# Optimization experiments

Hardware: AMD Instinct MI355X
Metric: run time of the kernel (lower is better)

## Reference

```python
import jax, jax.numpy as jnp
import numpy as np

B, C, H, W = 8, 256, 64, 64   # batch, num_hiddens, spatial
N, D = 1024, 256              # n_embed, embedding_dim
TEMP = 1.0                    # temp_init


def setup_inputs() -> dict:
    key = jax.random.key(0)
    k1, k2, k3 = jax.random.split(key, 3)
    z = jax.random.normal(k1, (B, C, H, W), dtype=jnp.float32)
    # 1x1 conv == per-pixel linear: weight [n_embed, num_hiddens], bias [n_embed]
    proj_w = jax.random.normal(k2, (N, C), dtype=jnp.float32) * 0.02
    proj_b = jnp.zeros((N,), dtype=jnp.float32)
    embed = jax.random.normal(k3, (N, D), dtype=jnp.float32) * 0.02
    return {"z": z, "proj_w": proj_w, "proj_b": proj_b, "embed": embed}


def reference(z, proj_w, proj_b, embed):
    # logits = Conv2d(num_hiddens, n_embed, 1)(z)  -> [b, n, h, w]
    logits = jnp.einsum('bchw,nc->bnhw', z, proj_w) + proj_b[None, :, None, None]
    # argmax_softmax (straight-through) over the codebook axis (dim=1), tau=TEMP
    y_soft = jax.nn.softmax(logits / TEMP, axis=1)
    ind = jnp.argmax(y_soft, axis=1)  # [b, h, w]
    y_hard = jax.nn.one_hot(ind, N, axis=1, dtype=logits.dtype)  # [b, n, h, w]
    soft_one_hot = y_hard - jax.lax.stop_gradient(y_soft) + y_soft
    # z_q = einsum('b n h w, n d -> b d h w', soft_one_hot, embed)
    z_q = jnp.einsum('bnhw,nd->bdhw', soft_one_hot, embed)
    diff = jnp.zeros((1,), dtype=logits.dtype)
    return (z_q, diff, ind)
```

## Files before the change

kernel.cpp:

```cpp
#include <hip/hip_runtime.h>
#include <math.h>

#define HWP 4096
#define CCH 256
#define NN  1024
#define DD  256
#define ZQ_SIZE (8 * DD * HWP)
#define MARGIN 1e-4f
#define WLCAP 4096

typedef _Float16 h8 __attribute__((ext_vector_type(8)));
typedef float    f4 __attribute__((ext_vector_type(4)));

__global__ __launch_bounds__(256) void split_w_k(
    const float* __restrict__ w, _Float16* __restrict__ whS, _Float16* __restrict__ wlS,
    int* __restrict__ wcount)
{
    if (blockIdx.x == 0 && threadIdx.x == 0) *wcount = 0;
    const int t = blockIdx.x * 256 + threadIdx.x;
    const int l = t & 63;
    const int frag = t >> 6;
    const int kc = frag & 7, r16 = frag >> 3;
    const int row = r16 * 16 + (l & 15);
    const int c   = kc * 32 + (l >> 4) * 8;
    const float* src = w + (size_t)row * CCH + c;
    _Float16 hv[8], lv[8];
#pragma unroll
    for (int j = 0; j < 8; ++j) {
        const float x = src[j];
        const _Float16 h = (_Float16)x;
        hv[j] = h;
        lv[j] = (_Float16)(x - (float)h);
    }
    *(h8*)(whS + (size_t)t * 8) = *(const h8*)hv;
    *(h8*)(wlS + (size_t)t * 8) = *(const h8*)lv;
}

__global__ __launch_bounds__(256, 2) void mfma_gemm_k(
    const float* __restrict__ z,
    const _Float16* __restrict__ whS, const _Float16* __restrict__ wlS,
    const float* __restrict__ bias, const float* __restrict__ embed,
    int* __restrict__ wcount, int* __restrict__ wlist,
    float* __restrict__ out)
{
    __shared__ __align__(16) char smem[68608];
    __shared__ int indsh2[64];
    float* s_best = (float*)(smem + 65536);
    float* s_sec  = (float*)(smem + 66560);
    int*   s_idx  = (int*)  (smem + 67584);

    const int tid = threadIdx.x;
    const int l   = tid & 63;
    const int wv  = tid >> 6;
    const int c15 = l & 15, g = l >> 4;
    const int pix0 = blockIdx.x * 64;
    const int b = pix0 >> 12, p0 = pix0 & 4095;

    {
        const int px = tid & 63;
        const int p16 = px >> 4;
        const float* zb = z + (size_t)b * CCH * HWP + p0 + px;
#pragma unroll
        for (int it = 0; it < 8; ++it) {
            const int cg = wv * 8 + it;
            const int c = cg * 8;
            float xv[8];
#pragma unroll
            for (int i = 0; i < 8; ++i) xv[i] = zb[(size_t)(c + i) * HWP];
            _Float16 hv[8], lv[8];
#pragma unroll
            for (int i = 0; i < 8; ++i) {
                const _Float16 h = (_Float16)xv[i];
                hv[i] = h;
                lv[i] = (_Float16)(xv[i] - (float)h);
            }
            const int kc = cg >> 2;
            const int lane = (px & 15) + 16 * (cg & 3);
            const int off = ((p16 * 8 + kc) * 64 + lane) * 16;
            *(h8*)(smem + off)         = *(const h8*)hv;
            *(h8*)(smem + 32768 + off) = *(const h8*)lv;
        }
    }
    __syncthreads();

    float best[16], sec[16]; int bidx[16];
#pragma unroll
    for (int s = 0; s < 16; ++s) { best[s] = -INFINITY; sec[s] = -INFINITY; bidx[s] = 0; }

#pragma unroll 1
    for (int nt = 0; nt < 4; ++nt) {
        const int n0 = nt * 256 + wv * 64;
        const int r16_0 = n0 >> 4;
        f4 acc[4][4];
#pragma unroll
        for (int mf = 0; mf < 4; ++mf)
#pragma unroll
            for (int nf = 0; nf < 4; ++nf) acc[mf][nf] = (f4)0.f;

#pragma unroll 2
        for (int kc = 0; kc < 8; ++kc) {
            h8 ah[4], al[4], bh[4], bl[4];
#pragma unroll
            for (int mf = 0; mf < 4; ++mf) {
                const int ao = ((mf * 8 + kc) * 64 + l) * 16;
                ah[mf] = *(const h8*)(smem + ao);
                al[mf] = *(const h8*)(smem + 32768 + ao);
            }
#pragma unroll
            for (int nf = 0; nf < 4; ++nf) {
                const size_t bo = (((size_t)(r16_0 + nf) * 8 + kc) * 64 + l) * 8;
                bh[nf] = *(const h8*)(whS + bo);
                bl[nf] = *(const h8*)(wlS + bo);
            }
#pragma unroll
            for (int mf = 0; mf < 4; ++mf)
#pragma unroll
                for (int nf = 0; nf < 4; ++nf) {
                    acc[mf][nf] = __builtin_amdgcn_mfma_f32_16x16x32_f16(ah[mf], bh[nf], acc[mf][nf], 0, 0, 0);
                    acc[mf][nf] = __builtin_amdgcn_mfma_f32_16x16x32_f16(ah[mf], bl[nf], acc[mf][nf], 0, 0, 0);
                    acc[mf][nf] = __builtin_amdgcn_mfma_f32_16x16x32_f16(al[mf], bh[nf], acc[mf][nf], 0, 0, 0);
                }
        }
#pragma unroll
        for (int nf = 0; nf < 4; ++nf) {
            const int n_abs = n0 + nf * 16 + c15;
            const float bv = bias[n_abs];
#pragma unroll
            for (int mf = 0; mf < 4; ++mf)
#pragma unroll
                for (int r = 0; r < 4; ++r) {
                    const float v = acc[mf][nf][r] + bv;
                    const int s = mf * 4 + r;
                    if (v > best[s]) { sec[s] = best[s]; best[s] = v; bidx[s] = n_abs; }
                    else if (v > sec[s]) sec[s] = v;
                }
        }
    }

#pragma unroll
    for (int d = 1; d < 16; d <<= 1) {
#pragma unroll
        for (int s = 0; s < 16; ++s) {
            const float ob = __shfl_xor(best[s], d, 64);
            const float os = __shfl_xor(sec[s], d, 64);
            const int   oi = __shfl_xor(bidx[s], d, 64);
            if (ob > best[s])       { sec[s] = fmaxf(best[s], os); best[s] = ob; bidx[s] = oi; }
            else if (ob == best[s]) { sec[s] = ob; bidx[s] = (oi < bidx[s]) ? oi : bidx[s]; }
            else                    { sec[s] = fmaxf(sec[s], ob); }
        }
    }
#pragma unroll
    for (int s = 0; s < 16; ++s) {
        if (c15 == s) {
            const int px = (s >> 2) * 16 + g * 4 + (s & 3);
            s_best[wv * 64 + px] = best[s];
            s_sec [wv * 64 + px] = sec[s];
            s_idx [wv * 64 + px] = bidx[s];
        }
    }
    __syncthreads();
    if (tid < 64) {
        float b0 = s_best[tid], s0 = s_sec[tid]; int i0 = s_idx[tid];
#pragma unroll
        for (int c = 1; c < 4; ++c) {
            const float ob = s_best[c * 64 + tid], os = s_sec[c * 64 + tid];
            const int   oi = s_idx[c * 64 + tid];
            if (ob > b0 || (ob == b0 && oi < i0)) { s0 = fmaxf(b0, os); b0 = ob; i0 = oi; }
            else                                  { s0 = fmaxf(s0, ob); }
        }
        const int pix = pix0 + tid;
        indsh2[tid] = i0;
        out[ZQ_SIZE + 1 + pix] = (float)i0;
        if (b0 - s0 < MARGIN) {
            const int pos = atomicAdd(wcount, 1);
            if (pos < WLCAP) wlist[pos] = pix;
        }
    }
    if (blockIdx.x == 0 && tid == 0) out[ZQ_SIZE] = 0.0f;
    __syncthreads();

    float (*tile)[257] = (float (*)[257])smem;
    const int lq = tid & 63, wq = tid >> 6;
    const int l32 = tid & 31, dq = tid >> 5;
#pragma unroll 1
    for (int pp = 0; pp < 2; ++pp) {
#pragma unroll
        for (int it = 0; it < 8; ++it) {
            const int pl = it * 4 + wq;
            const int row = indsh2[pp * 32 + pl];
            const float4 e = *(const float4*)(embed + (size_t)row * DD + lq * 4);
            tile[pl][lq * 4 + 0] = e.x;
            tile[pl][lq * 4 + 1] = e.y;
            tile[pl][lq * 4 + 2] = e.z;
            tile[pl][lq * 4 + 3] = e.w;
        }
        __syncthreads();
        float* outz = out + (size_t)b * DD * HWP + p0 + pp * 32;
#pragma unroll
        for (int dd = 0; dd < 32; ++dd) {
            const int d = dd * 8 + dq;
            outz[(size_t)d * HWP + l32] = tile[l32][d];
        }
        __syncthreads();
    }
}

__global__ __launch_bounds__(256) void fixup_k(
    const float* __restrict__ z, const float* __restrict__ w,
    const float* __restrict__ bias, const float* __restrict__ embed,
    const int* __restrict__ wcount, const int* __restrict__ wlist,
    float* __restrict__ out)
{
    __shared__ float zsh[256];
    __shared__ float m_v[4];
    __shared__ int   m_i[4];
    __shared__ int   s_i;

    const int tid = threadIdx.x;
    const int l = tid & 63, wv = tid >> 6;
    const int c15 = l & 15, q = l >> 4;
    int nw = *wcount;
    if (nw > WLCAP) nw = WLCAP;

    for (int e = blockIdx.x; e < nw; e += 256) {
        const int pix = wlist[e];
        const int b = pix >> 12, p = pix & 4095;
        __syncthreads();
        zsh[tid] = z[((size_t)b * CCH + tid) * HWP + p];
        __syncthreads();

        float best = -INFINITY; int bi = 0;
        for (int g16 = 0; g16 < 16; ++g16) {
            const int row = wv * 256 + g16 * 16 + c15;
            const float* wr = w + (size_t)row * CCH + q * 64;
            float part = 0.f;
#pragma unroll
            for (int j = 0; j < 16; ++j) {
                const float4 w4 = *(const float4*)(wr + j * 4);
                const float4 z4 = *(const float4*)&zsh[q * 64 + j * 4];
                part = fmaf(w4.x, z4.x, part);
                part = fmaf(w4.y, z4.y, part);
                part = fmaf(w4.z, z4.z, part);
                part = fmaf(w4.w, z4.w, part);
            }
            part += __shfl_xor(part, 16, 64);
            part += __shfl_xor(part, 32, 64);
            const float v = part + bias[row];
            if (v > best) { best = v; bi = row; }
        }
#pragma unroll
        for (int d = 1; d < 16; d <<= 1) {
            const float ob = __shfl_xor(best, d, 64);
            const int   oi = __shfl_xor(bi, d, 64);
            if (ob > best || (ob == best && oi < bi)) { best = ob; bi = oi; }
        }
        if (l == 0) { m_v[wv] = best; m_i[wv] = bi; }
        __syncthreads();
        if (tid == 0) {
            float v = m_v[0]; int i = m_i[0];
#pragma unroll
            for (int t = 1; t < 4; ++t)
                if (m_v[t] > v || (m_v[t] == v && m_i[t] < i)) { v = m_v[t]; i = m_i[t]; }
            s_i = i;
            out[ZQ_SIZE + 1 + pix] = (float)i;
        }
        __syncthreads();
        const int ii = s_i;
        out[((size_t)b * DD + tid) * HWP + p] = embed[(size_t)ii * DD + tid];
    }
}

extern "C" void kernel_launch(void* const* d_in, const int* in_sizes, int n_in,
                              void* d_out, int out_size, void* d_ws, size_t ws_size,
                              hipStream_t stream) {
    const float* z     = (const float*)d_in[0];
    const float* w     = (const float*)d_in[1];
    const float* bias  = (const float*)d_in[2];
    const float* embed = (const float*)d_in[3];
    float* out = (float*)d_out;

    _Float16* whS = (_Float16*)d_ws;
    _Float16* wlS = (_Float16*)((char*)d_ws + 524288);
    int* wcount = (int*)((char*)d_ws + 1048576);
    int* wlist  = (int*)((char*)d_ws + 1048832);

    hipLaunchKernelGGL(split_w_k,   dim3(128), dim3(256), 0, stream, w, whS, wlS, wcount);
    hipLaunchKernelGGL(mfma_gemm_k, dim3(512), dim3(256), 0, stream,
                       z, whS, wlS, bias, embed, wcount, wlist, out);
    hipLaunchKernelGGL(fixup_k,     dim3(256), dim3(256), 0, stream,
                       z, w, bias, embed, wcount, wlist, out);
}
```

Measured before the change: 187.9 us.

## Drop fp16 split-precision GEMM, widen fixup margin and fixup grid

Replaces the three-MFMA hi/lo fp16 split GEMM with a single plain fp16 MFMA, halving shared memory and raising launch bounds to 4 blocks per CU. To compensate for the lower accuracy, the argmax ambiguity margin grows from 1e-4 to 4e-3, so more pixels go to the exact fp32 fixup kernel, whose grid is widened to 2048 blocks. The risk is that many more pixels are flagged, and if the count exceeds WLCAP some near-ties would be left with fp16-only results.

```diff
diff --git a/kernel.cpp b/kernel.cpp
--- a/kernel.cpp
+++ b/kernel.cpp
@@ -6,14 +6,14 @@
 #define NN  1024
 #define DD  256
 #define ZQ_SIZE (8 * DD * HWP)
-#define MARGIN 1e-4f
+#define MARGIN 4e-3f
 #define WLCAP 4096
 
 typedef _Float16 h8 __attribute__((ext_vector_type(8)));
 typedef float    f4 __attribute__((ext_vector_type(4)));
 
 __global__ __launch_bounds__(256) void split_w_k(
-    const float* __restrict__ w, _Float16* __restrict__ whS, _Float16* __restrict__ wlS,
+    const float* __restrict__ w, _Float16* __restrict__ wS,
     int* __restrict__ wcount)
 {
     if (blockIdx.x == 0 && threadIdx.x == 0) *wcount = 0;
@@ -24,30 +24,24 @@
     const int row = r16 * 16 + (l & 15);
     const int c   = kc * 32 + (l >> 4) * 8;
     const float* src = w + (size_t)row * CCH + c;
-    _Float16 hv[8], lv[8];
-#pragma unroll
-    for (int j = 0; j < 8; ++j) {
-        const float x = src[j];
-        const _Float16 h = (_Float16)x;
-        hv[j] = h;
-        lv[j] = (_Float16)(x - (float)h);
-    }
-    *(h8*)(whS + (size_t)t * 8) = *(const h8*)hv;
-    *(h8*)(wlS + (size_t)t * 8) = *(const h8*)lv;
-}
-
-__global__ __launch_bounds__(256, 2) void mfma_gemm_k(
+    _Float16 hv[8];
+#pragma unroll
+    for (int j = 0; j < 8; ++j) hv[j] = (_Float16)src[j];
+    *(h8*)(wS + (size_t)t * 8) = *(const h8*)hv;
+}
+
+__global__ __launch_bounds__(256, 4) void mfma_gemm_k(
     const float* __restrict__ z,
-    const _Float16* __restrict__ whS, const _Float16* __restrict__ wlS,
+    const _Float16* __restrict__ wS,
     const float* __restrict__ bias, const float* __restrict__ embed,
     int* __restrict__ wcount, int* __restrict__ wlist,
     float* __restrict__ out)
 {
-    __shared__ __align__(16) char smem[68608];
+    __shared__ __align__(16) char smem[35840];
     __shared__ int indsh2[64];
-    float* s_best = (float*)(smem + 65536);
-    float* s_sec  = (float*)(smem + 66560);
-    int*   s_idx  = (int*)  (smem + 67584);
+    float* s_best = (float*)(smem + 32768);
+    float* s_sec  = (float*)(smem + 33792);
+    int*   s_idx  = (int*)  (smem + 34816);
 
     const int tid = threadIdx.x;
     const int l   = tid & 63;
@@ -67,18 +61,13 @@
             float xv[8];
 #pragma unroll
             for (int i = 0; i < 8; ++i) xv[i] = zb[(size_t)(c + i) * HWP];
-            _Float16 hv[8], lv[8];
-#pragma unroll
-            for (int i = 0; i < 8; ++i) {
-                const _Float16 h = (_Float16)xv[i];
-                hv[i] = h;
-                lv[i] = (_Float16)(xv[i] - (float)h);
-            }
+            _Float16 hv[8];
+#pragma unroll
+            for (int i = 0; i < 8; ++i) hv[i] = (_Float16)xv[i];
             const int kc = cg >> 2;
             const int lane = (px & 15) + 16 * (cg & 3);
             const int off = ((p16 * 8 + kc) * 64 + lane) * 16;
-            *(h8*)(smem + off)         = *(const h8*)hv;
-            *(h8*)(smem + 32768 + off) = *(const h8*)lv;
+            *(h8*)(smem + off) = *(const h8*)hv;
         }
     }
     __syncthreads();
@@ -99,27 +88,22 @@
 
 #pragma unroll 2
         for (int kc = 0; kc < 8; ++kc) {
-            h8 ah[4], al[4], bh[4], bl[4];
+            h8 ah[4], bh[4];
 #pragma unroll
             for (int mf = 0; mf < 4; ++mf) {
                 const int ao = ((mf * 8 + kc) * 64 + l) * 16;
                 ah[mf] = *(const h8*)(smem + ao);
-                al[mf] = *(const h8*)(smem + 32768 + ao);
             }
 #pragma unroll
             for (int nf = 0; nf < 4; ++nf) {
                 const size_t bo = (((size_t)(r16_0 + nf) * 8 + kc) * 64 + l) * 8;
-                bh[nf] = *(const h8*)(whS + bo);
-                bl[nf] = *(const h8*)(wlS + bo);
+                bh[nf] = *(const h8*)(wS + bo);
             }
 #pragma unroll
             for (int mf = 0; mf < 4; ++mf)
 #pragma unroll
-                for (int nf = 0; nf < 4; ++nf) {
+                for (int nf = 0; nf < 4; ++nf)
                     acc[mf][nf] = __builtin_amdgcn_mfma_f32_16x16x32_f16(ah[mf], bh[nf], acc[mf][nf], 0, 0, 0);
-                    acc[mf][nf] = __builtin_amdgcn_mfma_f32_16x16x32_f16(ah[mf], bl[nf], acc[mf][nf], 0, 0, 0);
-                    acc[mf][nf] = __builtin_amdgcn_mfma_f32_16x16x32_f16(al[mf], bh[nf], acc[mf][nf], 0, 0, 0);
-                }
         }
 #pragma unroll
         for (int nf = 0; nf < 4; ++nf) {
@@ -222,7 +206,7 @@
     int nw = *wcount;
     if (nw > WLCAP) nw = WLCAP;
 
-    for (int e = blockIdx.x; e < nw; e += 256) {
+    for (int e = blockIdx.x; e < nw; e += 2048) {
         const int pix = wlist[e];
         const int b = pix >> 12, p = pix & 4095;
         __syncthreads();
@@ -279,14 +263,13 @@
     const float* embed = (const float*)d_in[3];
     float* out = (float*)d_out;
 
-    _Float16* whS = (_Float16*)d_ws;
-    _Float16* wlS = (_Float16*)((char*)d_ws + 524288);
-    int* wcount = (int*)((char*)d_ws + 1048576);
-    int* wlist  = (int*)((char*)d_ws + 1048832);
-
-    hipLaunchKernelGGL(split_w_k,   dim3(128), dim3(256), 0, stream, w, whS, wlS, wcount);
+    _Float16* wS = (_Float16*)d_ws;
+    int* wcount = (int*)((char*)d_ws + 524288);
+    int* wlist  = (int*)((char*)d_ws + 524544);
+
+    hipLaunchKernelGGL(split_w_k,   dim3(128), dim3(256), 0, stream, w, wS, wcount);
     hipLaunchKernelGGL(mfma_gemm_k, dim3(512), dim3(256), 0, stream,
-                       z, whS, wlS, bias, embed, wcount, wlist, out);
-    hipLaunchKernelGGL(fixup_k,     dim3(256), dim3(256), 0, stream,
+                       z, wS, bias, embed, wcount, wlist, out);
+    hipLaunchKernelGGL(fixup_k,     dim3(2048), dim3(256), 0, stream,
                        z, w, bias, embed, wcount, wlist, out);
 }
```

Result: slower. 435.2 us (+131.6%).
